# Kernel optimization log

Hardware: AMD Instinct MI355X
Metric: run time of the kernel (lower is better)

Reference implementation:

```python
import jax, jax.numpy as jnp
import numpy as np

N = 100000
E = 1600000
D_IN = 128
D_OUT = 64


def setup_inputs() -> dict:
    key = jax.random.key(0)
    k1, k2, k3, k4, k5 = jax.random.split(key, 5)
    x = jax.random.normal(k1, (N, D_IN), dtype=jnp.float32)
    edge_row = jax.random.randint(k2, (E,), 0, N, dtype=jnp.int32)
    edge_col = jax.random.randint(k3, (E,), 0, N, dtype=jnp.int32)
    edge_val = jax.random.uniform(k4, (E,), dtype=jnp.float32)
    # Glorot-uniform init as in the torch module
    init_range = np.sqrt(6.0 / (D_IN + D_OUT))
    weight = jax.random.uniform(k5, (D_IN, D_OUT), dtype=jnp.float32,
                                minval=-init_range, maxval=init_range)
    return {"x": x, "edge_row": edge_row, "edge_col": edge_col,
            "edge_val": edge_val, "weight": weight}


def reference(x, edge_row, edge_col, edge_val, weight):
    # Dense projection: [N, D_in] @ [D_in, D_out] -> [N, D_out]
    xw = jnp.matmul(x, weight)
    # Sparse aggregation (SpMM with COO support): out[r] += val * xw[c]
    msgs = edge_val[:, None] * xw[edge_col]          # [E, D_out]
    out = jax.ops.segment_sum(msgs, edge_row, num_segments=x.shape[0])
    # bias=False, activation=relu
    return jax.nn.relu(out)
```

## Files before the change

kernel.cpp:

```cpp
#include <hip/hip_runtime.h>

#define NN 100000
#define DIN 128
#define DOUT 64
#define NE 1600000

#define BSHIFT 6
#define BROWS 64
#define NB 1563
#define CAP 1536
#define EPB 8192

#define XWB_B  0u
#define GCUR_B 12800000u
#define BPAD_B (GCUR_B + 8192u)
#define WS_NEED (BPAD_B + (unsigned)NB * CAP * 8u)

typedef unsigned short u16;
typedef unsigned int u32;
typedef __attribute__((ext_vector_type(8))) short v8s;
typedef __attribute__((ext_vector_type(4))) float v4f;

__device__ __forceinline__ float bf2f(u16 u) {
  return __uint_as_float(((u32)u) << 16);
}
__device__ __forceinline__ u16 f2bf(float f) {
  u32 x = __float_as_uint(f);
  u32 r = x + 0x7fffu + ((x >> 16) & 1u);
  return (u16)(r >> 16);
}

__global__ __launch_bounds__(256) void gemm_kernel(
    const float* __restrict__ x, const float* __restrict__ w,
    u16* __restrict__ xwb) {
  __shared__ u16 wlds[16 * 64 * 8];
  const int t = threadIdx.x;
  const int lane = t & 63;
  const int wv = t >> 6;

  #pragma unroll
  for (int pi = 0; pi < 4; ++pi) {
    const int p = t * 4 + pi;
    const int f = p >> 6, lp = p & 63;
    const int kc = f >> 2, nc = f & 3;
    const int kg = lp >> 4, lr = lp & 15;
    const int kbase = kc * 32 + kg * 8;
    u32 pk[4];
    #pragma unroll
    for (int h = 0; h < 4; ++h) {
      const u32 lo = f2bf(w[(kbase + 2 * h)     * DOUT + nc * 16 + lr]);
      const u32 hi = f2bf(w[(kbase + 2 * h + 1) * DOUT + nc * 16 + lr]);
      pk[h] = lo | (hi << 16);
    }
    *reinterpret_cast<uint4*>(&wlds[p * 8]) =
        make_uint4(pk[0], pk[1], pk[2], pk[3]);
  }
  __syncthreads();

  const int row0 = blockIdx.x * 64 + wv * 16;
  if (row0 >= NN) return;
  const int lrow = lane & 15;
  const int lkg  = lane >> 4;

  v8s Bf[4][4];
  #pragma unroll
  for (int kc = 0; kc < 4; ++kc)
    #pragma unroll
    for (int nc = 0; nc < 4; ++nc)
      Bf[kc][nc] = *reinterpret_cast<const v8s*>(
          &wlds[((kc * 4 + nc) * 64 + lane) * 8]);

  const float* xr = x + (size_t)(row0 + lrow) * DIN + lkg * 8;
  float4 xa[4][2];
  #pragma unroll
  for (int kc = 0; kc < 4; ++kc) {
    xa[kc][0] = *reinterpret_cast<const float4*>(xr + kc * 32);
    xa[kc][1] = *reinterpret_cast<const float4*>(xr + kc * 32 + 4);
  }

  v4f acc[4];
  #pragma unroll
  for (int nc = 0; nc < 4; ++nc) acc[nc] = (v4f){0.f, 0.f, 0.f, 0.f};

  #pragma unroll
  for (int kc = 0; kc < 4; ++kc) {
    v8s Af;
    Af[0] = (short)f2bf(xa[kc][0].x);
    Af[1] = (short)f2bf(xa[kc][0].y);
    Af[2] = (short)f2bf(xa[kc][0].z);
    Af[3] = (short)f2bf(xa[kc][0].w);
    Af[4] = (short)f2bf(xa[kc][1].x);
    Af[5] = (short)f2bf(xa[kc][1].y);
    Af[6] = (short)f2bf(xa[kc][1].z);
    Af[7] = (short)f2bf(xa[kc][1].w);
    #pragma unroll
    for (int nc = 0; nc < 4; ++nc)
      acc[nc] = __builtin_amdgcn_mfma_f32_16x16x32_bf16(Af, Bf[kc][nc],
                                                        acc[nc], 0, 0, 0);
  }

  #pragma unroll
  for (int nc = 0; nc < 4; ++nc)
    #pragma unroll
    for (int j = 0; j < 4; ++j)
      xwb[(size_t)(row0 + lkg * 4 + j) * DOUT + nc * 16 + lrow] =
          f2bf(acc[nc][j]);
}

__global__ __launch_bounds__(1024) void place_kernel(
    const int* __restrict__ erow, const int* __restrict__ ecol,
    const float* __restrict__ eval_, int* __restrict__ gcur,
    int2* __restrict__ bpad) {
  __shared__ int hist[NB];
  __shared__ int base[NB];
  __shared__ int lcur[NB];
  const int t = threadIdx.x;
  for (int i = t; i < NB; i += 1024) { hist[i] = 0; lcur[i] = 0; }
  __syncthreads();

  const int e0 = blockIdx.x * EPB;
  const int e1 = min(e0 + EPB, NE);
  for (int e = e0 + t; e < e1; e += 1024)
    atomicAdd(&hist[erow[e] >> BSHIFT], 1);
  __syncthreads();

  for (int i = t; i < NB; i += 1024) {
    const int h = hist[i];
    base[i] = h ? atomicAdd(&gcur[i], h) : 0;
  }
  __syncthreads();

  for (int e = e0 + t; e < e1; e += 1024) {
    const int r = erow[e];
    const int b = r >> BSHIFT;
    const int rank = base[b] + atomicAdd(&lcur[b], 1);
    if (rank < CAP) {
      int2 q;
      q.x = ((r & (BROWS - 1)) << 17) | ecol[e];
      q.y = __float_as_int(eval_[e]);
      bpad[(long)b * CAP + rank] = q;
    }
  }
}

__global__ __launch_bounds__(256) void agg2_kernel(
    const int* __restrict__ gcur, const int2* __restrict__ bpad,
    const u16* __restrict__ xwb, float* __restrict__ out) {
  __shared__ int2 dst[CAP];
  __shared__ int  hist[BROWS];
  __shared__ int  lptr[BROWS + 1];
  __shared__ int  cur[BROWS];

  const int bucket = blockIdx.x;
  const int t = threadIdx.x;
  const int count = min(gcur[bucket], CAP);
  const long sbase = (long)bucket * CAP;

  if (t < BROWS) hist[t] = 0;
  __syncthreads();

  int2 qr[6];
  #pragma unroll
  for (int k = 0; k < 6; ++k) {
    const int e = t + k * 256;
    if (e < count) {
      qr[k] = bpad[sbase + e];
      atomicAdd(&hist[(qr[k].x >> 17) & (BROWS - 1)], 1);
    }
  }
  __syncthreads();

  if (t < 64) {
    const int v = hist[t];
    int s = v;
    #pragma unroll
    for (int o = 1; o < 64; o <<= 1) {
      const int u = __shfl_up(s, o);
      if (t >= o) s += u;
    }
    lptr[t + 1] = s;
    cur[t] = s - v;
    if (t == 0) lptr[0] = 0;
  }
  __syncthreads();

  #pragma unroll
  for (int k = 0; k < 6; ++k) {
    const int e = t + k * 256;
    if (e < count) {
      const int r = (qr[k].x >> 17) & (BROWS - 1);
      const int pos = atomicAdd(&cur[r], 1);
      dst[pos] = qr[k];
    }
  }
  __syncthreads();

  const int lane = t & 63;
  const int wave = t >> 6;
  const int slot = lane >> 4;
  const int li   = lane & 15;
  const int row0 = bucket << BSHIFT;
  const int cmax = count - 1;

  for (int r = wave; r < BROWS; r += 4) {
    const int row = row0 + r;
    if (row >= NN) break;
    const int s = lptr[r], en = lptr[r + 1];
    float a0 = 0.f, a1 = 0.f, a2 = 0.f, a3 = 0.f;
    for (int e = s; e < en; e += 8) {
      {
        const int idx = e + slot;
        const int2 q = dst[min(idx, cmax)];
        const float v = (idx < en) ? __int_as_float(q.y) : 0.f;
        const u32 col = (u32)q.x & 0x1FFFFu;
        const uint2 g = *reinterpret_cast<const uint2*>(
            xwb + (size_t)col * DOUT + li * 4);
        a0 = fmaf(v, __uint_as_float(g.x << 16), a0);
        a1 = fmaf(v, __uint_as_float(g.x & 0xFFFF0000u), a1);
        a2 = fmaf(v, __uint_as_float(g.y << 16), a2);
        a3 = fmaf(v, __uint_as_float(g.y & 0xFFFF0000u), a3);
      }
      {
        const int idx = e + 4 + slot;
        const int2 q = dst[min(idx, cmax)];
        const float v = (idx < en) ? __int_as_float(q.y) : 0.f;
        const u32 col = (u32)q.x & 0x1FFFFu;
        const uint2 g = *reinterpret_cast<const uint2*>(
            xwb + (size_t)col * DOUT + li * 4);
        a0 = fmaf(v, __uint_as_float(g.x << 16), a0);
        a1 = fmaf(v, __uint_as_float(g.x & 0xFFFF0000u), a1);
        a2 = fmaf(v, __uint_as_float(g.y << 16), a2);
        a3 = fmaf(v, __uint_as_float(g.y & 0xFFFF0000u), a3);
      }
    }
    a0 += __shfl_xor(a0, 16); a0 += __shfl_xor(a0, 32);
    a1 += __shfl_xor(a1, 16); a1 += __shfl_xor(a1, 32);
    a2 += __shfl_xor(a2, 16); a2 += __shfl_xor(a2, 32);
    a3 += __shfl_xor(a3, 16); a3 += __shfl_xor(a3, 32);
    if (slot == 0) {
      float4 o;
      o.x = fmaxf(a0, 0.f); o.y = fmaxf(a1, 0.f);
      o.z = fmaxf(a2, 0.f); o.w = fmaxf(a3, 0.f);
      *reinterpret_cast<float4*>(&out[(size_t)row * DOUT + li * 4]) = o;
    }
  }
}

__global__ __launch_bounds__(256) void scatter_kernel(
    const int* __restrict__ erow, const int* __restrict__ ecol,
    const float* __restrict__ eval_, const u16* __restrict__ xwb,
    float* __restrict__ out) {
  const int wave = (blockIdx.x * blockDim.x + threadIdx.x) >> 6;
  const int lane = threadIdx.x & 63;
  const int nwaves = (gridDim.x * blockDim.x) >> 6;
  const int per = (NE + nwaves - 1) / nwaves;
  const int e0 = wave * per;
  const int e1 = min(e0 + per, NE);
  for (int base = e0; base < e1; base += 64) {
    const int e = base + lane;
    int r = 0, c = 0; float v = 0.f;
    if (e < e1) { r = erow[e]; c = ecol[e]; v = eval_[e]; }
    const int cnt = min(64, e1 - base);
    for (int j = 0; j < cnt; ++j) {
      const int rj = __shfl(r, j);
      const int cj = __shfl(c, j);
      const float vj = __shfl(v, j);
      atomicAdd(&out[rj * DOUT + lane], vj * bf2f(xwb[cj * DOUT + lane]));
    }
  }
}

__global__ __launch_bounds__(256) void finish_kernel(float* __restrict__ out) {
  const int idx = (blockIdx.x * blockDim.x + threadIdx.x) * 4;
  if (idx < NN * DOUT) {
    float4 a = *reinterpret_cast<const float4*>(&out[idx]);
    a.x = fmaxf(a.x, 0.f); a.y = fmaxf(a.y, 0.f);
    a.z = fmaxf(a.z, 0.f); a.w = fmaxf(a.w, 0.f);
    *reinterpret_cast<float4*>(&out[idx]) = a;
  }
}

extern "C" void kernel_launch(void* const* d_in, const int* in_sizes, int n_in,
                              void* d_out, int out_size, void* d_ws, size_t ws_size,
                              hipStream_t stream) {
  const float* x     = (const float*)d_in[0];
  const int*   erow  = (const int*)d_in[1];
  const int*   ecol  = (const int*)d_in[2];
  const float* eval_ = (const float*)d_in[3];
  const float* w     = (const float*)d_in[4];
  float* out = (float*)d_out;

  char* ws = (char*)d_ws;
  u16* xwb = (u16*)(ws + XWB_B);

  const int gemm_grid = (NN + 63) / 64;
  gemm_kernel<<<gemm_grid, 256, 0, stream>>>(x, w, xwb);

  if (ws_size >= (size_t)WS_NEED) {
    int*  gcur = (int*)(ws + GCUR_B);
    int2* bpad = (int2*)(ws + BPAD_B);

    hipMemsetAsync(gcur, 0, NB * 4, stream);
    const int place_grid = (NE + EPB - 1) / EPB;
    place_kernel<<<place_grid, 1024, 0, stream>>>(erow, ecol, eval_, gcur, bpad);
    agg2_kernel<<<NB, 256, 0, stream>>>(gcur, bpad, xwb, out);
  } else {
    hipMemsetAsync(d_out, 0, (size_t)NN * DOUT * sizeof(float), stream);
    scatter_kernel<<<2048, 256, 0, stream>>>(erow, ecol, eval_, xwb, out);
    const int fin_grid = (NN * DOUT / 4 + 255) / 256;
    finish_kernel<<<fin_grid, 256, 0, stream>>>(out);
  }
}
```

Measured before the change: 79.71 us.

## Replace global-atomic bucket placement with per-block local sort plus offset scan

The placement kernel now sorts each 8192-edge chunk by bucket inside shared memory and writes it out contiguously, so stores are coalesced and the global atomics on the bucket cursors are gone. A new scan kernel walks the 196 per-chunk offset tables for each bucket and builds segment records. The aggregation kernel then gathers those segments into shared memory before doing the per-row sort. This trades scattered global writes for an extra launch, a serial scan over 196 chunks per bucket, and a gather of many short runs in the aggregation step, where only 196 of the 256 threads do the loading.

```diff
diff --git a/kernel.cpp b/kernel.cpp
--- a/kernel.cpp
+++ b/kernel.cpp
@@ -10,11 +10,16 @@
 #define NB 1563
 #define CAP 1536
 #define EPB 8192
-
-#define XWB_B  0u
-#define GCUR_B 12800000u
-#define BPAD_B (GCUR_B + 8192u)
-#define WS_NEED (BPAD_B + (unsigned)NB * CAP * 8u)
+#define NBLK 196
+#define NBP 1568
+#define RECP 200
+
+#define XWB_B   0u
+#define SEG_B   12800000u
+#define LOFS_B  (SEG_B + 12845056u)
+#define RECT_B  (LOFS_B + 1229312u)
+#define GCUR2_B (RECT_B + 1250400u)
+#define WS_NEED (GCUR2_B + 6252u + 64u)
 
 typedef unsigned short u16;
 typedef unsigned int u32;
@@ -107,45 +112,99 @@
           f2bf(acc[nc][j]);
 }
 
-__global__ __launch_bounds__(1024) void place_kernel(
+__global__ __launch_bounds__(1024) void place2_kernel(
     const int* __restrict__ erow, const int* __restrict__ ecol,
-    const float* __restrict__ eval_, int* __restrict__ gcur,
-    int2* __restrict__ bpad) {
-  __shared__ int hist[NB];
-  __shared__ int base[NB];
+    const float* __restrict__ eval_, int2* __restrict__ seg,
+    int* __restrict__ lofs_g) {
+  __shared__ int hist[2048];
+  __shared__ int lofs[NB + 1];
   __shared__ int lcur[NB];
+  __shared__ int wtot[16];
+  __shared__ u16 sperm[EPB];
+
   const int t = threadIdx.x;
-  for (int i = t; i < NB; i += 1024) { hist[i] = 0; lcur[i] = 0; }
-  __syncthreads();
-
-  const int e0 = blockIdx.x * EPB;
+  const int lane = t & 63;
+  const int wv = t >> 6;
+  const int blk = blockIdx.x;
+  const int e0 = blk * EPB;
   const int e1 = min(e0 + EPB, NE);
+  const int ecount = e1 - e0;
+
+  for (int i = t; i < 2048; i += 1024) hist[i] = 0;
+  for (int i = t; i < NB; i += 1024) lcur[i] = 0;
+  __syncthreads();
+
   for (int e = e0 + t; e < e1; e += 1024)
     atomicAdd(&hist[erow[e] >> BSHIFT], 1);
   __syncthreads();
 
-  for (int i = t; i < NB; i += 1024) {
-    const int h = hist[i];
-    base[i] = h ? atomicAdd(&gcur[i], h) : 0;
-  }
+  const int ha = hist[2 * t], hb = hist[2 * t + 1];
+  const int ps = ha + hb;
+  int s = ps;
+  #pragma unroll
+  for (int o = 1; o < 64; o <<= 1) {
+    const int u = __shfl_up(s, o);
+    if (lane >= o) s += u;
+  }
+  if (lane == 63) wtot[wv] = s;
+  __syncthreads();
+  int woff = 0;
+  #pragma unroll
+  for (int w = 0; w < 16; ++w) woff += (w < wv) ? wtot[w] : 0;
+  const int excl = woff + s - ps;
+  if (2 * t     <= NB) lofs[2 * t]     = excl;
+  if (2 * t + 1 <= NB) lofs[2 * t + 1] = excl + ha;
   __syncthreads();
 
   for (int e = e0 + t; e < e1; e += 1024) {
-    const int r = erow[e];
-    const int b = r >> BSHIFT;
-    const int rank = base[b] + atomicAdd(&lcur[b], 1);
-    if (rank < CAP) {
+    const int b = erow[e] >> BSHIFT;
+    const int pos = lofs[b] + atomicAdd(&lcur[b], 1);
+    sperm[pos] = (u16)(e - e0);
+  }
+  __syncthreads();
+
+  for (int i = t; i < NB + 1; i += 1024)
+    lofs_g[(size_t)blk * NBP + i] = lofs[i];
+
+  #pragma unroll
+  for (int k = 0; k < 8; ++k) {
+    const int p = t + k * 1024;
+    if (p < ecount) {
+      const int e = e0 + sperm[p];
       int2 q;
-      q.x = ((r & (BROWS - 1)) << 17) | ecol[e];
+      q.x = ((erow[e] & (BROWS - 1)) << 17) | ecol[e];
       q.y = __float_as_int(eval_[e]);
-      bpad[(long)b * CAP + rank] = q;
-    }
-  }
-}
-
-__global__ __launch_bounds__(256) void agg2_kernel(
-    const int* __restrict__ gcur, const int2* __restrict__ bpad,
-    const u16* __restrict__ xwb, float* __restrict__ out) {
+      seg[(size_t)blk * EPB + p] = q;
+    }
+  }
+}
+
+__global__ __launch_bounds__(256) void scan_kernel(
+    const int* __restrict__ lofs_g, u32* __restrict__ rect,
+    int* __restrict__ gcur) {
+  const int b = blockIdx.x * 256 + threadIdx.x;
+  if (b >= NB) return;
+  int run = 0;
+  for (int blk = 0; blk < NBLK; ++blk) {
+    const int l0 = lofs_g[(size_t)blk * NBP + b];
+    const int l1 = lofs_g[(size_t)blk * NBP + b + 1];
+    int len = l1 - l0;
+    const int room = CAP - run;
+    int lc = len < room ? len : (room > 0 ? room : 0);
+    if (lc > 255) lc = 255;
+    const u32 rec = (lc > 0)
+        ? ((u32)l0 | ((u32)lc << 13) | ((u32)run << 21)) : 0u;
+    rect[(size_t)b * RECP + blk] = rec;
+    run += lc;
+  }
+  gcur[b] = run;
+}
+
+__global__ __launch_bounds__(256) void agg4_kernel(
+    const int* __restrict__ gcur, const u32* __restrict__ rect,
+    const int2* __restrict__ seg, const u16* __restrict__ xwb,
+    float* __restrict__ out) {
+  __shared__ int2 draw[CAP];
   __shared__ int2 dst[CAP];
   __shared__ int  hist[BROWS];
   __shared__ int  lptr[BROWS + 1];
@@ -153,19 +212,34 @@
 
   const int bucket = blockIdx.x;
   const int t = threadIdx.x;
-  const int count = min(gcur[bucket], CAP);
-  const long sbase = (long)bucket * CAP;
+  const int count = gcur[bucket];
 
   if (t < BROWS) hist[t] = 0;
   __syncthreads();
 
-  int2 qr[6];
-  #pragma unroll
-  for (int k = 0; k < 6; ++k) {
-    const int e = t + k * 256;
-    if (e < count) {
-      qr[k] = bpad[sbase + e];
-      atomicAdd(&hist[(qr[k].x >> 17) & (BROWS - 1)], 1);
+  if (t < NBLK) {
+    const u32 rec = rect[(size_t)bucket * RECP + t];
+    const int len = (int)((rec >> 13) & 0xFFu);
+    if (len) {
+      const int l0 = (int)(rec & 0x1FFFu);
+      const int base = (int)(rec >> 21);
+      const int2* sp = seg + (size_t)t * EPB + l0;
+      int j = 0;
+      for (; j + 4 <= len; j += 4) {
+        const int2 q0 = sp[j],     q1 = sp[j + 1];
+        const int2 q2 = sp[j + 2], q3 = sp[j + 3];
+        draw[base + j]     = q0; draw[base + j + 1] = q1;
+        draw[base + j + 2] = q2; draw[base + j + 3] = q3;
+        atomicAdd(&hist[(q0.x >> 17) & (BROWS - 1)], 1);
+        atomicAdd(&hist[(q1.x >> 17) & (BROWS - 1)], 1);
+        atomicAdd(&hist[(q2.x >> 17) & (BROWS - 1)], 1);
+        atomicAdd(&hist[(q3.x >> 17) & (BROWS - 1)], 1);
+      }
+      for (; j < len; ++j) {
+        const int2 q = sp[j];
+        draw[base + j] = q;
+        atomicAdd(&hist[(q.x >> 17) & (BROWS - 1)], 1);
+      }
     }
   }
   __syncthreads();
@@ -184,14 +258,11 @@
   }
   __syncthreads();
 
-  #pragma unroll
-  for (int k = 0; k < 6; ++k) {
-    const int e = t + k * 256;
-    if (e < count) {
-      const int r = (qr[k].x >> 17) & (BROWS - 1);
-      const int pos = atomicAdd(&cur[r], 1);
-      dst[pos] = qr[k];
-    }
+  for (int e = t; e < count; e += 256) {
+    const int2 q = draw[e];
+    const int r = (q.x >> 17) & (BROWS - 1);
+    const int pos = atomicAdd(&cur[r], 1);
+    dst[pos] = q;
   }
   __syncthreads();
 
@@ -297,13 +368,14 @@
   gemm_kernel<<<gemm_grid, 256, 0, stream>>>(x, w, xwb);
 
   if (ws_size >= (size_t)WS_NEED) {
-    int*  gcur = (int*)(ws + GCUR_B);
-    int2* bpad = (int2*)(ws + BPAD_B);
-
-    hipMemsetAsync(gcur, 0, NB * 4, stream);
-    const int place_grid = (NE + EPB - 1) / EPB;
-    place_kernel<<<place_grid, 1024, 0, stream>>>(erow, ecol, eval_, gcur, bpad);
-    agg2_kernel<<<NB, 256, 0, stream>>>(gcur, bpad, xwb, out);
+    int2* seg    = (int2*)(ws + SEG_B);
+    int*  lofs_g = (int*)(ws + LOFS_B);
+    u32*  rect   = (u32*)(ws + RECT_B);
+    int*  gcur   = (int*)(ws + GCUR2_B);
+
+    place2_kernel<<<NBLK, 1024, 0, stream>>>(erow, ecol, eval_, seg, lofs_g);
+    scan_kernel<<<(NB + 255) / 256, 256, 0, stream>>>(lofs_g, rect, gcur);
+    agg4_kernel<<<NB, 256, 0, stream>>>(gcur, rect, seg, xwb, out);
   } else {
     hipMemsetAsync(d_out, 0, (size_t)NN * DOUT * sizeof(float), stream);
     scatter_kernel<<<2048, 256, 0, stream>>>(erow, ecol, eval_, xwb, out);
```

Result: slower. 125.6 us (+57.6%).

## Stage bucketed edges in shared memory before writing them out contiguously

Applied to the files above, without the earlier changes.

The edge placement kernel now holds its 8192 row indices in registers and builds a block-local prefix scan over the bucket histogram. It sorts the packed edges by bucket into shared memory, then writes them to the global bucket arrays in a contiguous pass. Before, each edge was scattered straight to global memory at a random bucket slot. The goal is more coalesced global writes and one fewer reload of the row array, at the cost of much more shared memory (about 90KB) per block and extra barriers.

```diff
diff --git a/kernel.cpp b/kernel.cpp
--- a/kernel.cpp
+++ b/kernel.cpp
@@ -10,6 +10,7 @@
 #define NB 1563
 #define CAP 1536
 #define EPB 8192
+#define NBLK 196
 
 #define XWB_B  0u
 #define GCUR_B 12800000u
@@ -107,39 +108,80 @@
           f2bf(acc[nc][j]);
 }
 
-__global__ __launch_bounds__(1024) void place_kernel(
+__global__ __launch_bounds__(1024) void place3_kernel(
     const int* __restrict__ erow, const int* __restrict__ ecol,
     const float* __restrict__ eval_, int* __restrict__ gcur,
     int2* __restrict__ bpad) {
-  __shared__ int hist[NB];
-  __shared__ int base[NB];
-  __shared__ int lcur[NB];
+  __shared__ int  hist[2048];
+  __shared__ int  lofs[NB + 1];
+  __shared__ int  lcur[NB];
+  __shared__ int  base_[NB];
+  __shared__ int  wtot[16];
+  __shared__ u16  sb[EPB];
+  __shared__ int2 dstl[EPB];
+
   const int t = threadIdx.x;
-  for (int i = t; i < NB; i += 1024) { hist[i] = 0; lcur[i] = 0; }
-  __syncthreads();
-
-  const int e0 = blockIdx.x * EPB;
+  const int lane = t & 63;
+  const int wv = t >> 6;
+  const int blk = blockIdx.x;
+  const int e0 = blk * EPB;
   const int e1 = min(e0 + EPB, NE);
-  for (int e = e0 + t; e < e1; e += 1024)
-    atomicAdd(&hist[erow[e] >> BSHIFT], 1);
-  __syncthreads();
-
+  const int ecount = e1 - e0;
+
+  for (int i = t; i < 2048; i += 1024) hist[i] = 0;
+  for (int i = t; i < NB; i += 1024) lcur[i] = 0;
+  __syncthreads();
+
+  int er[8];
+  #pragma unroll
+  for (int k = 0; k < 8; ++k) {
+    const int e = e0 + t + k * 1024;
+    er[k] = (e < e1) ? erow[e] : -1;
+    if (er[k] >= 0) atomicAdd(&hist[er[k] >> BSHIFT], 1);
+  }
+  __syncthreads();
+
+  const int ha = hist[2 * t], hb = hist[2 * t + 1];
+  const int ps = ha + hb;
+  int s = ps;
+  #pragma unroll
+  for (int o = 1; o < 64; o <<= 1) {
+    const int u = __shfl_up(s, o);
+    if (lane >= o) s += u;
+  }
+  if (lane == 63) wtot[wv] = s;
+  __syncthreads();
+  int woff = 0;
+  #pragma unroll
+  for (int w = 0; w < 16; ++w) woff += (w < wv) ? wtot[w] : 0;
+  const int excl = woff + s - ps;
+  if (2 * t     <= NB) lofs[2 * t]     = excl;
+  if (2 * t + 1 <= NB) lofs[2 * t + 1] = excl + ha;
   for (int i = t; i < NB; i += 1024) {
     const int h = hist[i];
-    base[i] = h ? atomicAdd(&gcur[i], h) : 0;
-  }
-  __syncthreads();
-
-  for (int e = e0 + t; e < e1; e += 1024) {
-    const int r = erow[e];
-    const int b = r >> BSHIFT;
-    const int rank = base[b] + atomicAdd(&lcur[b], 1);
-    if (rank < CAP) {
+    base_[i] = h ? atomicAdd(&gcur[i], h) : 0;
+  }
+  __syncthreads();
+
+  #pragma unroll
+  for (int k = 0; k < 8; ++k) {
+    const int e = e0 + t + k * 1024;
+    if (er[k] >= 0) {
+      const int b = er[k] >> BSHIFT;
+      const int pos = lofs[b] + atomicAdd(&lcur[b], 1);
       int2 q;
-      q.x = ((r & (BROWS - 1)) << 17) | ecol[e];
+      q.x = ((er[k] & (BROWS - 1)) << 17) | ecol[e];
       q.y = __float_as_int(eval_[e]);
-      bpad[(long)b * CAP + rank] = q;
-    }
+      dstl[pos] = q;
+      sb[pos] = (u16)b;
+    }
+  }
+  __syncthreads();
+
+  for (int p = t; p < ecount; p += 1024) {
+    const int b = sb[p];
+    const int rk = base_[b] + (p - lofs[b]);
+    if (rk < CAP) bpad[(long)b * CAP + rk] = dstl[p];
   }
 }
 
@@ -301,8 +343,7 @@
     int2* bpad = (int2*)(ws + BPAD_B);
 
     hipMemsetAsync(gcur, 0, NB * 4, stream);
-    const int place_grid = (NE + EPB - 1) / EPB;
-    place_kernel<<<place_grid, 1024, 0, stream>>>(erow, ecol, eval_, gcur, bpad);
+    place3_kernel<<<NBLK, 1024, 0, stream>>>(erow, ecol, eval_, gcur, bpad);
     agg2_kernel<<<NB, 256, 0, stream>>>(gcur, bpad, xwb, out);
   } else {
     hipMemsetAsync(d_out, 0, (size_t)NN * DOUT * sizeof(float), stream);
```

New measurement: 73.89 us. 1.08x faster.
